# Performance work log

Hardware: AMD Instinct MI355X
Metric: run time of the kernel (lower is better)

The kernel has to match this reference:

```python
import jax, jax.numpy as jnp
import numpy as np

H = 8          # nhead
EPS_Z = 1e-6   # linear-attention normalizer eps
LN_EPS = 1e-5  # torch LayerNorm default


def _ln(x, g, b):
    m = x.mean(-1, keepdims=True)
    v = ((x - m) ** 2).mean(-1, keepdims=True)
    return (x - m) * jax.lax.rsqrt(v + LN_EPS) * g + b


def setup_inputs() -> dict:
    key = jax.random.key(0)
    ks = jax.random.split(key, 8)
    B, S, E, F = 4, 8192, 512, 2048
    s = 0.02
    return {
        "src": jax.random.normal(ks[0], (B, S, E), jnp.float32),
        "Wq": jax.random.normal(ks[1], (E, E), jnp.float32) * s,
        "bq": jnp.zeros((E,), jnp.float32),
        "Wk": jax.random.normal(ks[2], (E, E), jnp.float32) * s,
        "bk": jnp.zeros((E,), jnp.float32),
        "Wv": jax.random.normal(ks[3], (E, E), jnp.float32) * s,
        "bv": jnp.zeros((E,), jnp.float32),
        "Wo": jax.random.normal(ks[4], (E, E), jnp.float32) * s,
        "bo": jnp.zeros((E,), jnp.float32),
        "W1": jax.random.normal(ks[5], (E, F), jnp.float32) * s,
        "b1": jnp.zeros((F,), jnp.float32),
        "W2": jax.random.normal(ks[6], (F, E), jnp.float32) * s,
        "b2": jnp.zeros((E,), jnp.float32),
        "g1": jnp.ones((E,), jnp.float32),
        "be1": jnp.zeros((E,), jnp.float32),
        "g2": jnp.ones((E,), jnp.float32),
        "be2": jnp.zeros((E,), jnp.float32),
    }


def reference(src, Wq, bq, Wk, bk, Wv, bv, Wo, bo, W1, b1, W2, b2, g1, be1, g2, be2):
    B, S, E = src.shape
    Dh = E // H

    def heads(x):  # [B,S,E] -> [B,H,S,Dh]
        return x.reshape(B, S, H, Dh).transpose(0, 2, 1, 3)

    q = heads(src @ Wq + bq)
    k = heads(src @ Wk + bk)
    v = heads(src @ Wv + bv)

    qm = jax.nn.elu(q) + 1.0  # feature map: ELU+1
    km = jax.nn.elu(k) + 1.0

    kv = jnp.einsum("bhsd,bhse->bhde", km, v)          # [B,H,Dh,Dh]
    ksum = km.sum(axis=2)                               # [B,H,Dh]
    z = 1.0 / (jnp.einsum("bhsd,bhd->bhs", qm, ksum) + EPS_Z)
    attn = jnp.einsum("bhsd,bhde->bhse", qm, kv) * z[..., None]

    attn = attn.transpose(0, 2, 1, 3).reshape(B, S, E) @ Wo + bo
    x = _ln(src + attn, g1, be1)
    ff = jax.nn.relu(x @ W1 + b1) @ W2 + b2
    return _ln(x + ff, g2, be2)
```

## Files before the change

### kernel.cpp

```cpp
#include <hip/hip_runtime.h>
#include <hip/hip_bf16.h>

typedef __attribute__((ext_vector_type(8))) short bf16x8;
typedef __attribute__((ext_vector_type(4))) float f32x4;

__device__ inline ushort f2bf(float f) {
    uint u = __float_as_uint(f);
    u += 0x7fff + ((u >> 16) & 1);
    return (ushort)(u >> 16);
}
__device__ inline float bf2f(ushort h) {
    return __uint_as_float(((uint)h) << 16);
}

__device__ inline void gload16(const void* g, void* lds) {
    __builtin_amdgcn_global_load_lds(
        (const __attribute__((address_space(1))) void*)g,
        (__attribute__((address_space(3))) void*)lds, 16, 0, 0);
}

__global__ void conv_bf16(const float* __restrict__ in, ushort* __restrict__ out, int n4) {
    int i = blockIdx.x * 256 + threadIdx.x;
    if (i >= n4) return;
    float4 a = ((const float4*)in)[i];
    ushort4 o;
    o.x = f2bf(a.x); o.y = f2bf(a.y); o.z = f2bf(a.z); o.w = f2bf(a.w);
    ((ushort4*)out)[i] = o;
}

__global__ void wconv_t(const float* __restrict__ in, ushort* __restrict__ out, int K, int N) {
    __shared__ float tile[32][33];
    int kb = blockIdx.y * 32, nb = blockIdx.x * 32;
    int tx = threadIdx.x & 31, ty = threadIdx.x >> 5;
#pragma unroll
    for (int i = 0; i < 4; i++)
        tile[ty + i * 8][tx] = in[(size_t)(kb + ty + i * 8) * N + nb + tx];
    __syncthreads();
#pragma unroll
    for (int i = 0; i < 4; i++) {
        int n = nb + ty + i * 8, k = kb + tx;
        out[(size_t)n * K + k] = f2bf(tile[tx][ty + i * 8]);
    }
}

__global__ void biascat(const float* __restrict__ a, const float* __restrict__ b,
                        const float* __restrict__ c, float* __restrict__ o) {
    int i = blockIdx.x * 256 + threadIdx.x;
    if (i < 512) o[i] = a[i];
    else if (i < 1024) o[i] = b[i - 512];
    else if (i < 1536) o[i] = c[i - 1024];
}

template <int EPI>
__global__ __launch_bounds__(512, 2) void gemm256(
    const ushort* __restrict__ A, const ushort* __restrict__ Bt,
    const float* __restrict__ bias, const ushort* __restrict__ res16,
    ushort* __restrict__ out16, int M, int N, int K, int nbx) {
    extern __shared__ char smem[];
    const int t = threadIdx.x;
    const int w = t >> 6, l = t & 63;
    const int wr = w >> 2, wc = w & 3;
    const int nwg = gridDim.x;
    const int cpx = nwg >> 3;
    const int swz = (blockIdx.x & 7) * cpx + (blockIdx.x >> 3);
    const int bx = swz % nbx, by = swz / nbx;

    const int sc = (t & 3) ^ ((t >> 3) & 3);
    const ushort* gA0 = A + (size_t)(by * 256 + (t >> 2)) * K + sc * 8;
    const ushort* gA1 = gA0 + (size_t)128 * K;
    const ushort* gB0 = Bt + (size_t)(bx * 256 + (t >> 2)) * K + sc * 8;
    const ushort* gB1 = gB0 + (size_t)128 * K;

#define STAGE(kt)                                             \
    {                                                         \
        char* Lb = smem + ((kt) & 3) * 32768 + (w << 10);     \
        const int ko_ = (kt) * 32;                            \
        gload16(gA0 + ko_, Lb);                               \
        gload16(gA1 + ko_, Lb + 8192);                        \
        gload16(gB0 + ko_, Lb + 16384);                       \
        gload16(gB1 + ko_, Lb + 24576);                       \
    }

    f32x4 acc[8][4] = {};
    const int Kt = K >> 5;

    const int R0a = wr * 128 + (l & 15);
    const int offA = R0a * 64 + (((l >> 4) ^ ((R0a >> 1) & 3)) << 4);
    const int R0b = wc * 64 + (l & 15);
    const int offB = 16384 + R0b * 64 + (((l >> 4) ^ ((R0b >> 1) & 3)) << 4);

    STAGE(0); STAGE(1); STAGE(2);

#pragma unroll 1
    for (int kt = 0; kt < Kt; ++kt) {
        if (kt + 3 < Kt) STAGE(kt + 3);
        const int rem = Kt - 1 - kt;
        if (rem >= 3)      asm volatile("s_waitcnt vmcnt(12)" ::: "memory");
        else if (rem == 2) asm volatile("s_waitcnt vmcnt(8)" ::: "memory");
        else if (rem == 1) asm volatile("s_waitcnt vmcnt(4)" ::: "memory");
        else               asm volatile("s_waitcnt vmcnt(0)" ::: "memory");
        __builtin_amdgcn_s_barrier();
        __builtin_amdgcn_sched_barrier(0);

        const char* bufp = smem + (kt & 3) * 32768;
        bf16x8 a[8], b[4];
        b[0] = *(const bf16x8*)(bufp + offB);
        b[1] = *(const bf16x8*)(bufp + offB + 1024);
        b[2] = *(const bf16x8*)(bufp + offB + 2048);
        b[3] = *(const bf16x8*)(bufp + offB + 3072);
        a[0] = *(const bf16x8*)(bufp + offA);
        a[1] = *(const bf16x8*)(bufp + offA + 1024);
        __builtin_amdgcn_sched_barrier(0);
#pragma unroll
        for (int p = 0; p < 4; ++p) {
            if (p < 3) {
                a[2 * p + 2] = *(const bf16x8*)(bufp + offA + (2 * p + 2) * 1024);
                a[2 * p + 3] = *(const bf16x8*)(bufp + offA + (2 * p + 3) * 1024);
                __builtin_amdgcn_sched_barrier(0);
            }
            __builtin_amdgcn_s_setprio(1);
#pragma unroll
            for (int mm = 0; mm < 2; ++mm)
#pragma unroll
                for (int n = 0; n < 4; ++n)
                    acc[2 * p + mm][n] = __builtin_amdgcn_mfma_f32_16x16x32_bf16(
                        a[2 * p + mm], b[n], acc[2 * p + mm][n], 0, 0, 0);
            __builtin_amdgcn_s_setprio(0);
            __builtin_amdgcn_sched_barrier(0);
        }
        __builtin_amdgcn_s_barrier();
        __builtin_amdgcn_sched_barrier(0);
    }
#undef STAGE

    const int row0 = by * 256 + wr * 128 + ((l >> 4) << 2);
    const int col0 = bx * 256 + wc * 64 + (l & 15);
    const int seg = bx >> 1;
    const size_t segoff = (size_t)seg * M * 512;
    const int c511 = col0 & 511;
    float bv[4];
#pragma unroll
    for (int n = 0; n < 4; n++) bv[n] = bias[col0 + n * 16];
#pragma unroll
    for (int m = 0; m < 8; m++) {
#pragma unroll
        for (int r = 0; r < 4; r++) {
            const int row = row0 + m * 16 + r;
            const size_t base = (size_t)row * N + col0;
#pragma unroll
            for (int n = 0; n < 4; n++) {
                float vv = acc[m][n][r] + bv[n];
                if constexpr (EPI == 2) {
                    vv = vv > 0.f ? vv : 0.f;
                    out16[base + n * 16] = f2bf(vv);
                } else if constexpr (EPI == 3) {
                    vv += bf2f(res16[base + n * 16]);
                    out16[base + n * 16] = f2bf(vv);
                } else if constexpr (EPI == 4) {
                    if (seg < 2) vv = vv > 0.f ? vv + 1.f : __expf(vv);
                    out16[segoff + (size_t)row * 512 + c511 + n * 16] = f2bf(vv);
                } else {
                    out16[base + n * 16] = f2bf(vv);
                }
            }
        }
    }
}

__global__ __launch_bounds__(256) void kv_partial(
    const ushort* __restrict__ km, const ushort* __restrict__ v,
    float* __restrict__ kvp, float* __restrict__ ksump, int S) {
    __shared__ ushort kms[32 * 64];
    __shared__ ushort vs[32 * 64];
    const int t = threadIdx.x;
    const int bh = blockIdx.y, b = bh >> 3, h = bh & 7;
    const int d0 = (t >> 4) * 4, e0 = (t & 15) * 4;
    float acc[4][4] = {};
    float ks = 0.f;
    const int s_base = blockIdx.x * 512;
    const int r = t >> 3, c8 = (t & 7) * 8;
    for (int s0 = 0; s0 < 512; s0 += 32) {
        size_t grow = ((size_t)b * S + s_base + s0 + r) * 512 + h * 64 + c8;
        *(uint4*)&kms[r * 64 + c8] = *(const uint4*)&km[grow];
        *(uint4*)&vs[r * 64 + c8] = *(const uint4*)&v[grow];
        __syncthreads();
#pragma unroll 4
        for (int s = 0; s < 32; ++s) {
            ushort4 ka = *(const ushort4*)&kms[s * 64 + d0];
            ushort4 vb = *(const ushort4*)&vs[s * 64 + e0];
            float a0 = bf2f(ka.x), a1 = bf2f(ka.y), a2 = bf2f(ka.z), a3 = bf2f(ka.w);
            float b0 = bf2f(vb.x), b1 = bf2f(vb.y), b2 = bf2f(vb.z), b3 = bf2f(vb.w);
            acc[0][0] += a0 * b0; acc[0][1] += a0 * b1; acc[0][2] += a0 * b2; acc[0][3] += a0 * b3;
            acc[1][0] += a1 * b0; acc[1][1] += a1 * b1; acc[1][2] += a1 * b2; acc[1][3] += a1 * b3;
            acc[2][0] += a2 * b0; acc[2][1] += a2 * b1; acc[2][2] += a2 * b2; acc[2][3] += a2 * b3;
            acc[3][0] += a3 * b0; acc[3][1] += a3 * b1; acc[3][2] += a3 * b2; acc[3][3] += a3 * b3;
            if (t < 64) ks += bf2f(kms[s * 64 + t]);
        }
        __syncthreads();
    }
    float* dst = kvp + ((size_t)bh * 16 + blockIdx.x) * 4096;
#pragma unroll
    for (int i = 0; i < 4; i++)
#pragma unroll
        for (int j = 0; j < 4; j++)
            dst[(d0 + i) * 64 + e0 + j] = acc[i][j];
    if (t < 64) ksump[((size_t)bh * 16 + blockIdx.x) * 64 + t] = ks;
}

__global__ void kv_reduce(const float* __restrict__ kvp, const float* __restrict__ ksump,
                          ushort* __restrict__ kvt, float* __restrict__ ksum) {
    int i = blockIdx.x * 256 + threadIdx.x;
    if (i < 32 * 4096) {
        int bh = i >> 12, de = i & 4095;
        int d = de >> 6, e = de & 63;
        float s = 0.f;
#pragma unroll
        for (int c = 0; c < 16; ++c) s += kvp[((size_t)bh * 16 + c) * 4096 + de];
        kvt[(size_t)bh * 4096 + e * 64 + d] = f2bf(s);
    } else {
        int j = i - 32 * 4096;
        if (j < 32 * 64) {
            int bh = j >> 6, d = j & 63;
            float s = 0.f;
#pragma unroll
            for (int c = 0; c < 16; ++c) s += ksump[((size_t)bh * 16 + c) * 64 + d];
            ksum[j] = s;
        }
    }
}

__global__ __launch_bounds__(256) void attn_mfma(
    const ushort* __restrict__ qm, const ushort* __restrict__ kvt,
    const float* __restrict__ ksum, ushort* __restrict__ attnE, int S) {
    __shared__ ushort As[128 * 128];
    __shared__ ushort Bs[128 * 64];
    __shared__ float zbuf[128][2];
    __shared__ float ks2[128];
    const int t = threadIdx.x, w = t >> 6, l = t & 63;
    const int cx = blockIdx.x, by = blockIdx.y;
    const int b = (by * 128) / S;
    const int h0 = cx * 2;
    const size_t arow0 = (size_t)(by * 128) * 512 + cx * 128;

#pragma unroll
    for (int rd = 0; rd < 8; ++rd) {
        const ushort* g = qm + arow0 + (size_t)(rd * 16 + w * 4 + (l >> 4)) * 512 + (l & 15) * 8;
        gload16(g, (char*)As + rd * 4096 + w * 1024);
    }
    const ushort* kvbase = kvt + (size_t)(b * 8 + h0) * 4096;
#pragma unroll
    for (int rd = 0; rd < 4; ++rd) {
        const ushort* g = kvbase + (rd * 32 + w * 8 + (l >> 3)) * 64 + (l & 7) * 8;
        gload16(g, (char*)Bs + rd * 4096 + w * 1024);
    }
    if (t < 128) ks2[t] = ksum[(b * 8 + h0) * 64 + t];
    __syncthreads();

    {
        const int r = t >> 1, hh = t & 1;
        float den = 0.f;
#pragma unroll
        for (int d0 = 0; d0 < 64; d0 += 8) {
            bf16x8 qv = *(const bf16x8*)&As[r * 128 + hh * 64 + d0];
#pragma unroll
            for (int j = 0; j < 8; j++) den += bf2f((ushort)qv[j]) * ks2[hh * 64 + d0 + j];
        }
        zbuf[r][hh] = 1.0f / (den + 1e-6f);
    }

    const int wr = w >> 1, wc = w & 1;
    const int ar = wr * 64 + (l & 15);
    const int br = wc * 64 + (l & 15);
    const int ko = (l >> 4) * 8;
    f32x4 acc[4][4] = {};
#pragma unroll
    for (int ks_ = 0; ks_ < 2; ++ks_) {
        bf16x8 a[4], bb[4];
#pragma unroll
        for (int m = 0; m < 4; m++)
            a[m] = *(const bf16x8*)&As[(ar + m * 16) * 128 + wc * 64 + ks_ * 32 + ko];
#pragma unroll
        for (int n = 0; n < 4; n++)
            bb[n] = *(const bf16x8*)&Bs[(br + n * 16) * 64 + ks_ * 32 + ko];
#pragma unroll
        for (int m = 0; m < 4; m++)
#pragma unroll
            for (int n = 0; n < 4; n++)
                acc[m][n] = __builtin_amdgcn_mfma_f32_16x16x32_bf16(a[m], bb[n], acc[m][n], 0, 0, 0);
    }
    __syncthreads();

    const int row0l = wr * 64 + ((l >> 4) << 2);
    ushort* outbase = attnE + (size_t)(by * 128) * 512 + cx * 128;
#pragma unroll
    for (int n = 0; n < 4; n++) {
#pragma unroll
        for (int m = 0; m < 4; m++) {
#pragma unroll
            for (int r = 0; r < 4; r++) {
                int rl = row0l + m * 16 + r;
                float z = zbuf[rl][wc];
                outbase[(size_t)rl * 512 + wc * 64 + n * 16 + (l & 15)] = f2bf(acc[m][n][r] * z);
            }
        }
    }
}

template <int OUT32>
__global__ __launch_bounds__(256) void ln_bf16(
    const ushort* __restrict__ in, const float* __restrict__ g, const float* __restrict__ be,
    void* __restrict__ outp, int Mrows) {
    const int w = threadIdx.x >> 6, l = threadIdx.x & 63;
    const int row = blockIdx.x * 4 + w;
    if (row >= Mrows) return;
    const ushort* rp = in + (size_t)row * 512;
    uint4 u = *(const uint4*)&rp[l * 8];
    float x[8];
    x[0] = bf2f((ushort)(u.x & 0xffff)); x[1] = bf2f((ushort)(u.x >> 16));
    x[2] = bf2f((ushort)(u.y & 0xffff)); x[3] = bf2f((ushort)(u.y >> 16));
    x[4] = bf2f((ushort)(u.z & 0xffff)); x[5] = bf2f((ushort)(u.z >> 16));
    x[6] = bf2f((ushort)(u.w & 0xffff)); x[7] = bf2f((ushort)(u.w >> 16));
    float s = 0.f, ss = 0.f;
#pragma unroll
    for (int j = 0; j < 8; j++) { s += x[j]; ss += x[j] * x[j]; }
#pragma unroll
    for (int o = 1; o < 64; o <<= 1) {
        s += __shfl_xor(s, o, 64);
        ss += __shfl_xor(ss, o, 64);
    }
    float mean = s * (1.f / 512.f);
    float var = ss * (1.f / 512.f) - mean * mean;
    float rstd = rsqrtf(var + 1e-5f);
    float4 g0 = *(const float4*)&g[l * 8], g1v = *(const float4*)&g[l * 8 + 4];
    float4 b0 = *(const float4*)&be[l * 8], b1v = *(const float4*)&be[l * 8 + 4];
    float o0[8];
    o0[0] = (x[0] - mean) * rstd * g0.x + b0.x;
    o0[1] = (x[1] - mean) * rstd * g0.y + b0.y;
    o0[2] = (x[2] - mean) * rstd * g0.z + b0.z;
    o0[3] = (x[3] - mean) * rstd * g0.w + b0.w;
    o0[4] = (x[4] - mean) * rstd * g1v.x + b1v.x;
    o0[5] = (x[5] - mean) * rstd * g1v.y + b1v.y;
    o0[6] = (x[6] - mean) * rstd * g1v.z + b1v.z;
    o0[7] = (x[7] - mean) * rstd * g1v.w + b1v.w;
    if constexpr (OUT32) {
        float* op = (float*)outp + (size_t)row * 512;
        *(float4*)&op[l * 8] = make_float4(o0[0], o0[1], o0[2], o0[3]);
        *(float4*)&op[l * 8 + 4] = make_float4(o0[4], o0[5], o0[6], o0[7]);
    } else {
        ushort* op = (ushort*)outp + (size_t)row * 512;
        ushort4 u0, u1;
        u0.x = f2bf(o0[0]); u0.y = f2bf(o0[1]); u0.z = f2bf(o0[2]); u0.w = f2bf(o0[3]);
        u1.x = f2bf(o0[4]); u1.y = f2bf(o0[5]); u1.z = f2bf(o0[6]); u1.w = f2bf(o0[7]);
        *(ushort4*)&op[l * 8] = u0;
        *(ushort4*)&op[l * 8 + 4] = u1;
    }
}

extern "C" void kernel_launch(void* const* d_in, const int* in_sizes, int n_in,
                              void* d_out, int out_size, void* d_ws, size_t ws_size,
                              hipStream_t stream) {
    const int B = 4, S = 8192, E = 512, F = 2048;
    const int M = B * S;
    const size_t SZ = (size_t)M * E * 2;
    const int SMEM = 131072;

    const float* src = (const float*)d_in[0];
    const float* Wq = (const float*)d_in[1];  const float* bq = (const float*)d_in[2];
    const float* Wk = (const float*)d_in[3];  const float* bk = (const float*)d_in[4];
    const float* Wv = (const float*)d_in[5];  const float* bv = (const float*)d_in[6];
    const float* Wo = (const float*)d_in[7];  const float* bo = (const float*)d_in[8];
    const float* W1 = (const float*)d_in[9];  const float* b1 = (const float*)d_in[10];
    const float* W2 = (const float*)d_in[11]; const float* b2 = (const float*)d_in[12];
    const float* g1 = (const float*)d_in[13]; const float* be1 = (const float*)d_in[14];
    const float* g2 = (const float*)d_in[15]; const float* be2 = (const float*)d_in[16];

    char* ws = (char*)d_ws;
    ushort* qm    = (ushort*)(ws + 0 * SZ);
    ushort* km    = (ushort*)(ws + 1 * SZ);
    ushort* v     = (ushort*)(ws + 2 * SZ);
    ushort* src16 = (ushort*)(ws + 3 * SZ);
    ushort* x16   = (ushort*)(ws + 4 * SZ);
    ushort* z16   = (ushort*)(ws + 5 * SZ);
    char*   tail  = ws + 6 * SZ;
    float*  kvp   = (float*)(tail);
    float*  ksump = (float*)(tail + 8388608);
    ushort* kvt   = (ushort*)(tail + 8519680);
    float*  ksum  = (float*)(tail + 8781824);
    float*  bqkv  = (float*)(tail + 8790016);
    ushort* wqkv  = (ushort*)(tail + 8796160);
    ushort* wot   = (ushort*)(tail + 10369024);
    ushort* w1t   = (ushort*)(tail + 10893312);
    ushort* w2t   = (ushort*)(tail + 12990464);
    ushort* attnE = km;
    ushort* y16   = v;
    ushort* hbuf  = (ushort*)(ws + 0);

    hipFuncSetAttribute((const void*)gemm256<2>, hipFuncAttributeMaxDynamicSharedMemorySize, SMEM);
    hipFuncSetAttribute((const void*)gemm256<3>, hipFuncAttributeMaxDynamicSharedMemorySize, SMEM);
    hipFuncSetAttribute((const void*)gemm256<4>, hipFuncAttributeMaxDynamicSharedMemorySize, SMEM);

    conv_bf16<<<dim3((M * E / 4 + 255) / 256), 256, 0, stream>>>(src, src16, M * E / 4);
    wconv_t<<<dim3(E / 32, E / 32), 256, 0, stream>>>(Wq, wqkv, E, E);
    wconv_t<<<dim3(E / 32, E / 32), 256, 0, stream>>>(Wk, wqkv + 512 * 512, E, E);
    wconv_t<<<dim3(E / 32, E / 32), 256, 0, stream>>>(Wv, wqkv + 1024 * 512, E, E);
    wconv_t<<<dim3(E / 32, E / 32), 256, 0, stream>>>(Wo, wot, E, E);
    wconv_t<<<dim3(F / 32, E / 32), 256, 0, stream>>>(W1, w1t, E, F);
    wconv_t<<<dim3(E / 32, F / 32), 256, 0, stream>>>(W2, w2t, F, E);
    biascat<<<dim3(6), 256, 0, stream>>>(bq, bk, bv, bqkv);

    gemm256<4><<<dim3(6 * 128), 512, SMEM, stream>>>(src16, wqkv, bqkv, nullptr, qm, M, 1536, E, 6);

    kv_partial<<<dim3(16, 32), 256, 0, stream>>>(km, v, kvp, ksump, S);
    kv_reduce<<<dim3((32 * 4096 + 32 * 64 + 255) / 256), 256, 0, stream>>>(kvp, ksump, kvt, ksum);

    attn_mfma<<<dim3(4, M / 128), 256, 0, stream>>>(qm, kvt, ksum, attnE, S);

    gemm256<3><<<dim3(2 * 128), 512, SMEM, stream>>>(attnE, wot, bo, src16, y16, M, E, E, 2);
    ln_bf16<0><<<dim3(M / 4), 256, 0, stream>>>(y16, g1, be1, x16, M);

    gemm256<2><<<dim3(8 * 128), 512, SMEM, stream>>>(x16, w1t, b1, nullptr, hbuf, M, F, E, 8);
    gemm256<3><<<dim3(2 * 128), 512, SMEM, stream>>>(hbuf, w2t, b2, x16, z16, M, E, F, 2);
    ln_bf16<1><<<dim3(M / 4), 256, 0, stream>>>(z16, g2, be2, (float*)d_out, M);
}
```

Before: 398.1 us.

## Split GEMM K-loop into two half-phases interleaving global prefetch with MFMA

Reworks the 256x256 bf16 GEMM main loop so each k-tile runs as two phases. Each phase issues half of the next-stage global-to-LDS loads, reads a group of A fragments, synchronizes with a barrier, then runs 16 MFMAs. The aim is to spread memory issue across the compute and hide LDS read latency, in the style of ping-pong scheduling. It adds an extra barrier per iteration and reorders the vmcnt waits, which may add stalls or race risk if the counts are off.

```diff
diff --git a/kernel.cpp b/kernel.cpp
--- a/kernel.cpp
+++ b/kernel.cpp
@@ -71,13 +71,18 @@
     const ushort* gB0 = Bt + (size_t)(bx * 256 + (t >> 2)) * K + sc * 8;
     const ushort* gB1 = gB0 + (size_t)128 * K;
 
-#define STAGE(kt)                                             \
+#define STAGE_H0(kt)                                          \
     {                                                         \
         char* Lb = smem + ((kt) & 3) * 32768 + (w << 10);     \
         const int ko_ = (kt) * 32;                            \
         gload16(gA0 + ko_, Lb);                               \
+        gload16(gB0 + ko_, Lb + 16384);                       \
+    }
+#define STAGE_H1(kt)                                          \
+    {                                                         \
+        char* Lb = smem + ((kt) & 3) * 32768 + (w << 10);     \
+        const int ko_ = (kt) * 32;                            \
         gload16(gA1 + ko_, Lb + 8192);                        \
-        gload16(gB0 + ko_, Lb + 16384);                       \
         gload16(gB1 + ko_, Lb + 24576);                       \
     }
 
@@ -89,14 +94,14 @@
     const int R0b = wc * 64 + (l & 15);
     const int offB = 16384 + R0b * 64 + (((l >> 4) ^ ((R0b >> 1) & 3)) << 4);
 
-    STAGE(0); STAGE(1); STAGE(2);
+    STAGE_H0(0); STAGE_H1(0);
+    STAGE_H0(1); STAGE_H1(1);
+    STAGE_H0(2); STAGE_H1(2);
 
 #pragma unroll 1
     for (int kt = 0; kt < Kt; ++kt) {
-        if (kt + 3 < Kt) STAGE(kt + 3);
         const int rem = Kt - 1 - kt;
-        if (rem >= 3)      asm volatile("s_waitcnt vmcnt(12)" ::: "memory");
-        else if (rem == 2) asm volatile("s_waitcnt vmcnt(8)" ::: "memory");
+        if (rem >= 2)      asm volatile("s_waitcnt vmcnt(8)" ::: "memory");
         else if (rem == 1) asm volatile("s_waitcnt vmcnt(4)" ::: "memory");
         else               asm volatile("s_waitcnt vmcnt(0)" ::: "memory");
         __builtin_amdgcn_s_barrier();
@@ -110,28 +115,41 @@
         b[3] = *(const bf16x8*)(bufp + offB + 3072);
         a[0] = *(const bf16x8*)(bufp + offA);
         a[1] = *(const bf16x8*)(bufp + offA + 1024);
-        __builtin_amdgcn_sched_barrier(0);
-#pragma unroll
-        for (int p = 0; p < 4; ++p) {
-            if (p < 3) {
-                a[2 * p + 2] = *(const bf16x8*)(bufp + offA + (2 * p + 2) * 1024);
-                a[2 * p + 3] = *(const bf16x8*)(bufp + offA + (2 * p + 3) * 1024);
-                __builtin_amdgcn_sched_barrier(0);
-            }
-            __builtin_amdgcn_s_setprio(1);
-#pragma unroll
-            for (int mm = 0; mm < 2; ++mm)
-#pragma unroll
-                for (int n = 0; n < 4; ++n)
-                    acc[2 * p + mm][n] = __builtin_amdgcn_mfma_f32_16x16x32_bf16(
-                        a[2 * p + mm], b[n], acc[2 * p + mm][n], 0, 0, 0);
-            __builtin_amdgcn_s_setprio(0);
-            __builtin_amdgcn_sched_barrier(0);
-        }
+        a[2] = *(const bf16x8*)(bufp + offA + 2048);
+        a[3] = *(const bf16x8*)(bufp + offA + 3072);
+        if (kt + 3 < Kt) STAGE_H0(kt + 3);
+        __builtin_amdgcn_sched_barrier(0);
         __builtin_amdgcn_s_barrier();
-        __builtin_amdgcn_sched_barrier(0);
-    }
-#undef STAGE
+        asm volatile("s_waitcnt lgkmcnt(0)" ::: "memory");
+        __builtin_amdgcn_sched_barrier(0);
+        __builtin_amdgcn_s_setprio(1);
+#pragma unroll
+        for (int m = 0; m < 4; m++)
+#pragma unroll
+            for (int n = 0; n < 4; n++)
+                acc[m][n] = __builtin_amdgcn_mfma_f32_16x16x32_bf16(a[m], b[n], acc[m][n], 0, 0, 0);
+        __builtin_amdgcn_s_setprio(0);
+        __builtin_amdgcn_sched_barrier(0);
+        a[4] = *(const bf16x8*)(bufp + offA + 4096);
+        a[5] = *(const bf16x8*)(bufp + offA + 5120);
+        a[6] = *(const bf16x8*)(bufp + offA + 6144);
+        a[7] = *(const bf16x8*)(bufp + offA + 7168);
+        if (kt + 3 < Kt) STAGE_H1(kt + 3);
+        __builtin_amdgcn_sched_barrier(0);
+        __builtin_amdgcn_s_barrier();
+        asm volatile("s_waitcnt lgkmcnt(0)" ::: "memory");
+        __builtin_amdgcn_sched_barrier(0);
+        __builtin_amdgcn_s_setprio(1);
+#pragma unroll
+        for (int m = 4; m < 8; m++)
+#pragma unroll
+            for (int n = 0; n < 4; n++)
+                acc[m][n] = __builtin_amdgcn_mfma_f32_16x16x32_bf16(a[m], b[n], acc[m][n], 0, 0, 0);
+        __builtin_amdgcn_s_setprio(0);
+        __builtin_amdgcn_sched_barrier(0);
+    }
+#undef STAGE_H0
+#undef STAGE_H1
 
     const int row0 = by * 256 + wr * 128 + ((l >> 4) << 2);
     const int col0 = bx * 256 + wc * 64 + (l & 15);
```

New measurement: 382.8 us. -3.8%, faster.
